# Optimization experiments

Measured on AMD Instinct MI355X. Metric: run time of the kernel, lower is better.

The kernel has to match this reference:

```python
import jax, jax.numpy as jnp
import numpy as np

B, N, C = 1, 32768, 256
NH, F, AG, P = 8, 32, 64, 4  # heads, cube side, agent tokens, pool size (P**3==AG)
HD = C // NH


def setup_inputs() -> dict:
    key = jax.random.key(0)
    ks = jax.random.split(key, 4)
    s = 0.02
    return {
        "x": jax.random.normal(ks[0], (B, N, C), jnp.float32),
        "w_qkv": jax.random.normal(ks[1], (3 * C, C), jnp.float32) * s,
        "b_qkv": jnp.zeros((3 * C,), jnp.float32),
        "w_proj": jax.random.normal(ks[2], (C, C), jnp.float32) * s,
        "b_proj": jnp.zeros((C,), jnp.float32),
        "w_dwc": jax.random.normal(ks[3], (C, C, 3, 3, 3), jnp.float32) * s,
        "b_dwc": jnp.zeros((C,), jnp.float32),
    }


def reference(x, w_qkv, b_qkv, w_proj, b_proj, w_dwc, b_dwc):
    scale = HD ** -0.5
    # qkv projection -> (3, B*NH, N, HD), replicating torch reshape/permute exactly
    qkv = x @ w_qkv.T + b_qkv                       # (B, N, 3C)
    qkv = qkv.reshape(B, N, 3, NH, HD)
    qkv = jnp.transpose(qkv, (2, 0, 3, 1, 4)).reshape(3, B * NH, N, HD)
    q, k, v = qkv[0], qkv[1], qkv[2]

    # agent tokens: pool q (note torch's raw reshape interleaves heads into channels)
    q_vol = q.reshape(B, F, F, F, C)                # faithful to torch reshape
    q_vol = jnp.transpose(q_vol, (0, 4, 1, 2, 3))   # (B, C, F, F, F)
    blk = F // P
    A = q_vol.reshape(B, C, P, blk, P, blk, P, blk).mean(axis=(3, 5, 7))  # (B,C,P,P,P)
    A = A.reshape(B, C, AG).transpose(0, 2, 1)      # (B, AG, C)
    A = A.reshape(B, AG, NH, HD).transpose(0, 2, 1, 3).reshape(B * NH, AG, HD)

    # stage 1: agents attend to keys, aggregate values
    agent_attn = jax.nn.softmax((A * scale) @ jnp.swapaxes(k, -2, -1), axis=-1)  # (B*NH, AG, N)
    agent_v = agent_attn @ v                        # (B*NH, AG, HD)
    # stage 2: queries attend to agents
    q_attn = jax.nn.softmax((q * scale) @ jnp.swapaxes(A, -2, -1), axis=-1)      # (B*NH, N, AG)
    o = q_attn @ agent_v                            # (B*NH, N, HD)

    # faithful to torch: transpose(1,2) then raw reshape
    o = jnp.swapaxes(o, 1, 2).reshape(B, N, C)

    # conv residual on v: (B*NH, N, HD) -> (B, C, F, F, F)
    v5 = jnp.swapaxes(v, 1, 2).reshape(B, C, F, F, F)
    conv = jax.lax.conv_general_dilated(
        v5, w_dwc, window_strides=(1, 1, 1), padding="SAME",
        dimension_numbers=("NCDHW", "OIDHW", "NCDHW"))
    conv = conv + b_dwc[None, :, None, None, None]
    o = o + jnp.transpose(conv, (0, 2, 3, 4, 1)).reshape(B, N, C)

    return o @ w_proj.T + b_proj
```

## Files before the change

kernel.cpp:

```cpp
#include <hip/hip_runtime.h>
#include <stdint.h>

typedef unsigned short u16;
typedef __attribute__((ext_vector_type(8))) short bf16x8;
typedef __attribute__((ext_vector_type(4))) float f32x4;

#define KSCALE (0.17677669529663687f / 512.0f)

__device__ __forceinline__ u16 f2b(float f) {
  unsigned u = __float_as_uint(f);
  unsigned r = (u + 0x7fffu + ((u >> 16) & 1u)) >> 16;
  return (u16)r;
}
__device__ __forceinline__ float b2f(u16 s) { return __uint_as_float(((unsigned)s) << 16); }

__device__ __forceinline__ void async16(const void* g, void* l) {
  __builtin_amdgcn_global_load_lds((const __attribute__((address_space(1))) unsigned int*)g,
                                   (__attribute__((address_space(3))) unsigned int*)l, 16, 0, 0);
}

__device__ __forceinline__ bf16x8 frag8(const float* p, float k) {
  float4 f0 = *(const float4*)p, f1 = *(const float4*)(p + 4);
  bf16x8 v;
  v[0] = f2b(f0.x * k); v[1] = f2b(f0.y * k); v[2] = f2b(f0.z * k); v[3] = f2b(f0.w * k);
  v[4] = f2b(f1.x * k); v[5] = f2b(f1.y * k); v[6] = f2b(f1.z * k); v[7] = f2b(f1.w * k);
  return v;
}

__global__ void prep_cast(const float* __restrict__ x, const float* __restrict__ wq,
                          const float* __restrict__ wp, const float* __restrict__ wdwc,
                          u16* __restrict__ Xb, u16* __restrict__ Wqb,
                          u16* __restrict__ Wpb, u16* __restrict__ Wc) {
  int b = blockIdx.x, tid = threadIdx.x;
  if (b < 8448) {
    const float* src; u16* dst; int i;
    if (b < 8192)      { src = x;  dst = Xb;  i = b * 256 + tid; }
    else if (b < 8384) { src = wq; dst = Wqb; i = (b - 8192) * 256 + tid; }
    else               { src = wp; dst = Wpb; i = (b - 8384) * 256 + tid; }
    const float4 v = ((const float4*)src)[i];
    uint2 o;
    o.x = (unsigned)f2b(v.x) | ((unsigned)f2b(v.y) << 16);
    o.y = (unsigned)f2b(v.z) | ((unsigned)f2b(v.w) << 16);
    ((uint2*)dst)[i] = o;
  } else {
    int o = b - 8448;
    __shared__ u16 lds[6912];
    for (int t = tid; t < 6912; t += 256) lds[t] = f2b(wdwc[o * 6912 + t]);
    __syncthreads();
    for (int idx = tid; idx < 6912; idx += 256) {
      int tp = idx >> 8, i = idx & 255;
      Wc[o * 6912 + idx] = lds[i * 27 + tp];
    }
  }
}

__global__ void prep_av(const u16* __restrict__ QKV, u16* __restrict__ v5,
                        float* __restrict__ Apre) {
  int b = blockIdx.x, tid = threadIdx.x;
  if (b < 4913) {
    int idx = b * 256 + tid;
    int c8 = idx & 31, vox = idx >> 5;
    int z = vox / 1156, r2 = vox - z * 1156, y = r2 / 34, x = r2 - y * 34;
    bf16x8 val = {0, 0, 0, 0, 0, 0, 0, 0};
    if (z >= 1 && z <= 32 && y >= 1 && y <= 32 && x >= 1 && x <= 32) {
      int n = (z - 1) * 1024 + (y - 1) * 32 + (x - 1);
      val = *(const bf16x8*)(QKV + n * 768 + 512 + c8 * 8);
    }
    *(bf16x8*)(v5 + vox * 256 + c8 * 8) = val;
  } else {
    int b2 = b - 4913;
    int a = b2 >> 3, s = b2 & 7;
    int hp = tid >> 5, dp = tid & 31;
    int p1 = a >> 4, p2 = (a >> 2) & 3, p3 = a & 3;
    float sum = 0.f;
    for (int ui = 0; ui < 64; ++ui) {
      int u = s * 64 + ui;
      int f1 = p1 * 8 + (u >> 6);
      int f2 = p2 * 8 + ((u >> 3) & 7);
      int f3 = p3 * 8 + (u & 7);
      int vox = f1 * 1024 + f2 * 32 + f3;
      int n  = ((vox & 4095) << 3) + hp;
      int cq = ((vox >> 12) << 5) + dp;
      sum += b2f(QKV[n * 768 + cq]);
    }
    atomicAdd(&Apre[(hp * 64 + a) * 32 + dp], sum);
  }
}


__device__ __forceinline__ void stage64(const u16* src, int row0, int ld, int k0,
                                        short* dst, int tid) {
  int wv = tid >> 6, lane = tid & 63;
  int r15 = lane & 15, kc8 = (lane >> 4) * 8;
#pragma unroll
  for (int j = 0; j < 4; ++j) {
    int p = j & 1, g = wv * 2 + (j >> 1);
    async16(src + (row0 + g * 16 + r15) * ld + k0 + p * 32 + kc8, dst + p * 4096 + g * 512);
  }
}

__device__ __forceinline__ void mfma64(const short* As, const short* Bs, int wm, int wn,
                                       int lane, f32x4 acc[4][4]) {
  const int q = lane >> 4, c = lane & 15;
  const int fo = q * 128 + c * 8;
#pragma unroll
  for (int p = 0; p < 2; ++p) {
    bf16x8 a[4], b[4];
#pragma unroll
    for (int mt = 0; mt < 4; ++mt) a[mt] = *(const bf16x8*)&As[p * 4096 + (wm * 4 + mt) * 512 + fo];
#pragma unroll
    for (int nt = 0; nt < 4; ++nt) b[nt] = *(const bf16x8*)&Bs[p * 4096 + (wn * 4 + nt) * 512 + fo];
#pragma unroll
    for (int mt = 0; mt < 4; ++mt)
#pragma unroll
      for (int nt = 0; nt < 4; ++nt)
        acc[mt][nt] = __builtin_amdgcn_mfma_f32_16x16x32_bf16(a[mt], b[nt], acc[mt][nt], 0, 0, 0);
  }
}

__global__ __launch_bounds__(256) void gemm_qkv(const u16* __restrict__ Xb,
                                                const u16* __restrict__ Wq,
                                                const float* __restrict__ bias,
                                                u16* __restrict__ QKV) {
  const int m0 = blockIdx.x * 128, n0 = blockIdx.y * 128;
  const int tid = threadIdx.x, lane = tid & 63, wv = tid >> 6;
  const int wm = wv >> 1, wn = wv & 1, q = lane >> 4, c = lane & 15;
  __shared__ short As[8192], Bs[8192];
  f32x4 acc[4][4] = {};
  for (int kb = 0; kb < 256; kb += 64) {
    stage64(Xb, m0, 256, kb, As, tid);
    stage64(Wq, n0, 256, kb, Bs, tid);
    __syncthreads();
    mfma64(As, Bs, wm, wn, lane, acc);
    __syncthreads();
  }
#pragma unroll
  for (int nt = 0; nt < 4; ++nt) {
    int col = n0 + wn * 64 + nt * 16 + c;
    float bv = bias[col];
#pragma unroll
    for (int mt = 0; mt < 4; ++mt) {
      int row = m0 + wm * 64 + mt * 16 + q * 4;
#pragma unroll
      for (int r = 0; r < 4; ++r) QKV[(row + r) * 768 + col] = f2b(acc[mt][nt][r] + bv);
    }
  }
}

__global__ __launch_bounds__(256) void conv_s1(const u16* __restrict__ v5,
                                               const u16* __restrict__ Wc,
                                               const float* __restrict__ bias,
                                               u16* __restrict__ Xp,
                                               const u16* __restrict__ QKV,
                                               const float* __restrict__ Apre,
                                               float* __restrict__ avac,
                                               float* __restrict__ rsum) {
  extern __shared__ char smem[];
  const int tid = threadIdx.x, lane = tid & 63, wv = tid >> 6;
  const int q = lane >> 4, c = lane & 15;
  if (blockIdx.x < 512) {
    const int bid = blockIdx.x;
    const int xcd = bid & 7, idx = bid >> 3;
    const int n0 = (idx & 1) * 128;
    const int mt_i = xcd * 32 + (idx >> 1);
    const int m0 = mt_i * 128;
    const int z0 = mt_i >> 3, y0 = (mt_i & 7) * 4;
    const int wm = wv >> 1, wn = wv & 1;
    const int r15 = lane & 15, kq8 = (lane >> 4) * 8;
    short* As = (short*)smem;
    short* Bs = (short*)(smem + 9216);
    f32x4 acc[4][4] = {};
    const u16* browB = Wc + (n0 + r15) * 6912 + kq8;
    for (int dzy = 0; dzy < 9; ++dzy) {
      int dz = dzy / 3, dy = dzy - dz * 3;
      int base = (z0 + dz) * 1156 + (y0 + dy) * 34;
      int tap0 = dzy * 3;
      for (int panel = 0; panel < 8; ++panel) {
        int choff = panel * 32 + kq8;
        for (int g = wv; g < 9; g += 4) {
          int row = base + g * 16 + r15;
          row = row < 39303 ? row : 39303;
          async16(v5 + row * 256 + choff, As + g * 512);
        }
#pragma unroll
        for (int i = wv; i < 24; i += 4) {
          int dx = i >> 3, g = i & 7;
          async16(browB + g * (16 * 6912) + (tap0 + dx) * 256 + panel * 32, Bs + i * 512);
        }
        __syncthreads();
#pragma unroll
        for (int dx = 0; dx < 3; ++dx) {
          bf16x8 a[4], b[4];
#pragma unroll
          for (int mt = 0; mt < 4; ++mt) {
            int M = wm * 64 + mt * 16 + c;
            int vx = M + 2 * (M >> 5) + dx;
            a[mt] = *(const bf16x8*)&As[(vx >> 4) * 512 + q * 128 + (vx & 15) * 8];
          }
#pragma unroll
          for (int nt = 0; nt < 4; ++nt)
            b[nt] = *(const bf16x8*)&Bs[dx * 4096 + (wn * 4 + nt) * 512 + q * 128 + c * 8];
#pragma unroll
          for (int mt = 0; mt < 4; ++mt)
#pragma unroll
            for (int nt = 0; nt < 4; ++nt)
              acc[mt][nt] = __builtin_amdgcn_mfma_f32_16x16x32_bf16(a[mt], b[nt], acc[mt][nt], 0, 0, 0);
        }
        __syncthreads();
      }
    }
#pragma unroll
    for (int nt = 0; nt < 4; ++nt) {
      int col = n0 + wn * 64 + nt * 16 + c;
      float bv = bias[col];
#pragma unroll
      for (int mt = 0; mt < 4; ++mt) {
        int row = m0 + wm * 64 + mt * 16 + q * 4;
#pragma unroll
        for (int r = 0; r < 4; ++r) Xp[(row + r) * 256 + col] = f2b(acc[mt][nt][r] + bv);
      }
    }
  } else {
    const int vb = blockIdx.x - 512;
    const int h = vb >> 7, n0 = (vb & 127) * 256;
    u16* E  = (u16*)smem;
    u16* VT = (u16*)(smem + 33792);
    float* RED = (float*)smem;
    {
      const u16* vrow = QKV + (n0 + tid) * 768 + 512 + h * 32;
#pragma unroll
      for (int d8 = 0; d8 < 4; ++d8) {
        bf16x8 v = *(const bf16x8*)(vrow + d8 * 8);
#pragma unroll
        for (int e = 0; e < 8; ++e) VT[(d8 * 8 + e) * 264 + tid] = (u16)v[e];
      }
    }
    {
      bf16x8 af[4], bf[4];
#pragma unroll
      for (int mt = 0; mt < 4; ++mt)
        af[mt] = frag8(Apre + h * 2048 + (mt * 16 + c) * 32 + q * 8, KSCALE);
#pragma unroll
      for (int nt = 0; nt < 4; ++nt)
        bf[nt] = *(const bf16x8*)(QKV + (n0 + wv * 64 + nt * 16 + c) * 768 + 256 + h * 32 + q * 8);
#pragma unroll
      for (int mt = 0; mt < 4; ++mt)
#pragma unroll
        for (int nt = 0; nt < 4; ++nt) {
          f32x4 s = {0.f, 0.f, 0.f, 0.f};
          s = __builtin_amdgcn_mfma_f32_16x16x32_bf16(af[mt], bf[nt], s, 0, 0, 0);
#pragma unroll
          for (int r = 0; r < 4; ++r) {
            int a = mt * 16 + q * 4 + r, nl = wv * 64 + nt * 16 + c;
            E[a * 264 + nl] = f2b(__expf(s[r]));
          }
        }
    }
    __syncthreads();
    {
      int a = tid >> 2, seg = tid & 3;
      float sum = 0.f;
      for (int i = 0; i < 64; ++i) sum += b2f(E[a * 264 + seg * 64 + i]);
      sum += __shfl_xor(sum, 1);
      sum += __shfl_xor(sum, 2);
      if (seg == 0) atomicAdd(&rsum[h * 64 + a], sum);
    }
    f32x4 pv[4][2] = {};
#pragma unroll
    for (int ks = 0; ks < 2; ++ks) {
      bf16x8 ap[4], bp[2];
#pragma unroll
      for (int mt = 0; mt < 4; ++mt)
        ap[mt] = *(const bf16x8*)&E[(mt * 16 + c) * 264 + wv * 64 + ks * 32 + q * 8];
#pragma unroll
      for (int nt = 0; nt < 2; ++nt)
        bp[nt] = *(const bf16x8*)&VT[(nt * 16 + c) * 264 + wv * 64 + ks * 32 + q * 8];
#pragma unroll
      for (int mt = 0; mt < 4; ++mt)
#pragma unroll
        for (int nt = 0; nt < 2; ++nt)
          pv[mt][nt] = __builtin_amdgcn_mfma_f32_16x16x32_bf16(ap[mt], bp[nt], pv[mt][nt], 0, 0, 0);
    }
    __syncthreads();
#pragma unroll
    for (int mt = 0; mt < 4; ++mt)
#pragma unroll
      for (int nt = 0; nt < 2; ++nt)
#pragma unroll
        for (int r = 0; r < 4; ++r)
          RED[wv * 2048 + (mt * 16 + q * 4 + r) * 32 + nt * 16 + c] = pv[mt][nt][r];
    __syncthreads();
    for (int idx = tid; idx < 2048; idx += 256) {
      float t = RED[idx] + RED[2048 + idx] + RED[4096 + idx] + RED[6144 + idx];
      atomicAdd(&avac[h * 2048 + idx], t);
    }
  }
}

__global__ __launch_bounds__(256) void gemm_proj(const u16* __restrict__ Xp,
                                                 const u16* __restrict__ Wp,
                                                 const float* __restrict__ bias,
                                                 float* __restrict__ out) {
  const int m0 = blockIdx.x * 128, n0 = blockIdx.y * 128;
  const int tid = threadIdx.x, lane = tid & 63, wv = tid >> 6;
  const int wm = wv >> 1, wn = wv & 1, q = lane >> 4, c = lane & 15;
  __shared__ short As[8192], Bs[8192];
  f32x4 acc[4][4] = {};
  for (int kb = 0; kb < 256; kb += 64) {
    stage64(Xp, m0, 256, kb, As, tid);
    stage64(Wp, n0, 256, kb, Bs, tid);
    __syncthreads();
    mfma64(As, Bs, wm, wn, lane, acc);
    __syncthreads();
  }
#pragma unroll
  for (int nt = 0; nt < 4; ++nt) {
    int col = n0 + wn * 64 + nt * 16 + c;
    float bv = bias[col];
#pragma unroll
    for (int mt = 0; mt < 4; ++mt) {
      int row = m0 + wm * 64 + mt * 16 + q * 4;
#pragma unroll
      for (int r = 0; r < 4; ++r) out[(row + r) * 256 + col] = acc[mt][nt][r] + bv;
    }
  }
}

__global__ __launch_bounds__(256) void s2_attn(const u16* __restrict__ QKV,
                                               const float* __restrict__ Apre,
                                               const float* __restrict__ avac,
                                               const float* __restrict__ rsum,
                                               u16* __restrict__ Xp) {
  const int h = blockIdx.y, n0 = blockIdx.x * 256;
  const int tid = threadIdx.x, lane = tid & 63, wv = tid >> 6;
  const int q = lane >> 4, c = lane & 15;
  extern __shared__ char smem[];
  u16* P = (u16*)smem;
  float* O = (float*)smem;
  u16* AVT = (u16*)(smem + 36864);

  for (int j = 0; j < 8; ++j) {
    int i = j * 256 + tid;
    int a = i >> 5, d = i & 31;
    AVT[d * 72 + a] = f2b(avac[h * 2048 + i] / rsum[h * 64 + a]);
  }

  f32x4 s[4][4];
  {
    bf16x8 af[4], bf[4];
#pragma unroll
    for (int mt = 0; mt < 4; ++mt)
      af[mt] = *(const bf16x8*)(QKV + (n0 + wv * 64 + mt * 16 + c) * 768 + h * 32 + q * 8);
#pragma unroll
    for (int nt = 0; nt < 4; ++nt)
      bf[nt] = frag8(Apre + h * 2048 + (nt * 16 + c) * 32 + q * 8, KSCALE);
#pragma unroll
    for (int mt = 0; mt < 4; ++mt)
#pragma unroll
      for (int nt = 0; nt < 4; ++nt) {
        f32x4 z = {0.f, 0.f, 0.f, 0.f};
        s[mt][nt] = __builtin_amdgcn_mfma_f32_16x16x32_bf16(af[mt], bf[nt], z, 0, 0, 0);
      }
  }
#pragma unroll
  for (int mt = 0; mt < 4; ++mt)
#pragma unroll
    for (int r = 0; r < 4; ++r) {
      float v0 = s[mt][0][r], v1 = s[mt][1][r], v2 = s[mt][2][r], v3 = s[mt][3][r];
      float mx = fmaxf(fmaxf(v0, v1), fmaxf(v2, v3));
      mx = fmaxf(mx, __shfl_xor(mx, 1));
      mx = fmaxf(mx, __shfl_xor(mx, 2));
      mx = fmaxf(mx, __shfl_xor(mx, 4));
      mx = fmaxf(mx, __shfl_xor(mx, 8));
      float e0 = __expf(v0 - mx), e1 = __expf(v1 - mx), e2 = __expf(v2 - mx), e3 = __expf(v3 - mx);
      float sm = e0 + e1 + e2 + e3;
      sm += __shfl_xor(sm, 1);
      sm += __shfl_xor(sm, 2);
      sm += __shfl_xor(sm, 4);
      sm += __shfl_xor(sm, 8);
      float inv = 1.0f / sm;
      int tok = wv * 64 + mt * 16 + q * 4 + r;
      P[tok * 72 +      c] = f2b(e0 * inv);
      P[tok * 72 + 16 + c] = f2b(e1 * inv);
      P[tok * 72 + 32 + c] = f2b(e2 * inv);
      P[tok * 72 + 48 + c] = f2b(e3 * inv);
    }
  __syncthreads();
  f32x4 o[4][2] = {};
#pragma unroll
  for (int ks = 0; ks < 2; ++ks) {
    bf16x8 ap[4], bv[2];
#pragma unroll
    for (int mt = 0; mt < 4; ++mt)
      ap[mt] = *(const bf16x8*)&P[(wv * 64 + mt * 16 + c) * 72 + ks * 32 + q * 8];
#pragma unroll
    for (int nt = 0; nt < 2; ++nt)
      bv[nt] = *(const bf16x8*)&AVT[(nt * 16 + c) * 72 + ks * 32 + q * 8];
#pragma unroll
    for (int mt = 0; mt < 4; ++mt)
#pragma unroll
      for (int nt = 0; nt < 2; ++nt)
        o[mt][nt] = __builtin_amdgcn_mfma_f32_16x16x32_bf16(ap[mt], bv[nt], o[mt][nt], 0, 0, 0);
  }
  __syncthreads();
#pragma unroll
  for (int mt = 0; mt < 4; ++mt)
#pragma unroll
    for (int nt = 0; nt < 2; ++nt)
#pragma unroll
      for (int r = 0; r < 4; ++r)
        O[(nt * 16 + c) * 258 + wv * 64 + mt * 16 + q * 4 + r] = o[mt][nt][r];
  __syncthreads();
  for (int d = 0; d < 32; ++d) {
    int addr = (h * 32 + d) * 32768 + n0 + tid;
    Xp[addr] = f2b(b2f(Xp[addr]) + O[d * 258 + tid]);
  }
}


extern "C" void kernel_launch(void* const* d_in, const int* in_sizes, int n_in,
                              void* d_out, int out_size, void* d_ws, size_t ws_size,
                              hipStream_t stream) {
  const float* x      = (const float*)d_in[0];
  const float* w_qkv  = (const float*)d_in[1];
  const float* b_qkv  = (const float*)d_in[2];
  const float* w_proj = (const float*)d_in[3];
  const float* b_proj = (const float*)d_in[4];
  const float* w_dwc  = (const float*)d_in[5];
  const float* b_dwc  = (const float*)d_in[6];
  float* out = (float*)d_out;
  char* ws = (char*)d_ws;

  u16* Xb   = (u16*)(ws);
  u16* QKV  = (u16*)(ws + 16777216);
  u16* V5   = (u16*)(ws + 67108864);
  u16* Wc   = (u16*)(ws + 87232512);
  u16* Wqb  = (u16*)(ws + 90771456);
  u16* Wpb  = (u16*)(ws + 91164672);
  float* AVAC = (float*)(ws + 91361280);
  float* RSUM = (float*)(ws + 91426816);
  float* APRE = (float*)(ws + 91428864);
  u16* Xp = Xb;

  hipMemsetAsync(AVAC, 0, 65536 + 2048 + 65536, stream);
  prep_cast<<<8704, 256, 0, stream>>>(x, w_qkv, w_proj, w_dwc, Xb, Wqb, Wpb, Wc);
  gemm_qkv<<<dim3(256, 6), 256, 0, stream>>>(Xb, Wqb, b_qkv, QKV);
  prep_av<<<5425, 256, 0, stream>>>(QKV, V5, APRE);
  conv_s1<<<2560, 256, 50688, stream>>>(V5, Wc, b_dwc, Xp, QKV, APRE, AVAC, RSUM);
  s2_attn<<<dim3(128, 8), 256, 41472, stream>>>(QKV, APRE, AVAC, RSUM, Xp);
  gemm_proj<<<dim3(256, 2), 256, 0, stream>>>(Xp, Wpb, b_proj, out);
}
```

Before: 349.1 us.

## Double-buffer conv A tiles and load pre-swizzled conv weights directly to registers

The conv-weight prep kernel now writes weights in an MFMA-fragment-friendly blocked layout, so the conv GEMM reads B fragments straight from global memory into registers instead of staging them through LDS. The A (voxel) tile is double-buffered in LDS, with the next step's async loads issued before the current step's MFMAs, leaving one barrier per step instead of two. This aims to hide global load latency and cut LDS traffic and syncs. In exchange it adds direct global loads on the critical path each step, which depend on L2 hits for the weights, and it raises register pressure.

```diff
diff --git a/kernel.cpp b/kernel.cpp
--- a/kernel.cpp
+++ b/kernel.cpp
@@ -47,9 +47,10 @@
     __shared__ u16 lds[6912];
     for (int t = tid; t < 6912; t += 256) lds[t] = f2b(wdwc[o * 6912 + t]);
     __syncthreads();
+    int ob = ((o >> 4) * 27) * 4096 + (o & 15) * 32;
     for (int idx = tid; idx < 6912; idx += 256) {
-      int tp = idx >> 8, i = idx & 255;
-      Wc[o * 6912 + idx] = lds[i * 27 + tp];
+      int t = idx >> 8, i = idx & 255;
+      Wc[ob + t * 4096 + (i >> 5) * 512 + ((i >> 3) & 3) * 8 + (i & 7)] = lds[i * 27 + t];
     }
   }
 }
@@ -167,47 +168,58 @@
     const int z0 = mt_i >> 3, y0 = (mt_i & 7) * 4;
     const int wm = wv >> 1, wn = wv & 1;
     const int r15 = lane & 15, kq8 = (lane >> 4) * 8;
-    short* As = (short*)smem;
-    short* Bs = (short*)(smem + 9216);
+    short* As0 = (short*)smem;
+    short* As1 = (short*)smem + 4608;
     f32x4 acc[4][4] = {};
-    const u16* browB = Wc + (n0 + r15) * 6912 + kq8;
-    for (int dzy = 0; dzy < 9; ++dzy) {
-      int dz = dzy / 3, dy = dzy - dz * 3;
-      int base = (z0 + dz) * 1156 + (y0 + dy) * 34;
-      int tap0 = dzy * 3;
-      for (int panel = 0; panel < 8; ++panel) {
-        int choff = panel * 32 + kq8;
+    const u16* Bq = Wc + c * 32 + q * 8;
+    const int nb = ((n0 >> 4) + wn * 4) * 27;
+    {
+      int base = z0 * 1156 + y0 * 34;
+      for (int g = wv; g < 9; g += 4) {
+        int row = base + g * 16 + r15;
+        row = row < 39303 ? row : 39303;
+        async16(v5 + row * 256 + kq8, As0 + g * 512);
+      }
+    }
+    __syncthreads();
+    short* cur = As0; short* nxt = As1;
+    for (int t = 0; t < 72; ++t) {
+      const int dzy = t >> 3, panel = t & 7;
+      const int tap0 = dzy * 3;
+      bf16x8 breg[3][4];
+#pragma unroll
+      for (int dx = 0; dx < 3; ++dx)
+#pragma unroll
+        for (int nt = 0; nt < 4; ++nt)
+          breg[dx][nt] = *(const bf16x8*)(Bq + ((nb + nt * 27 + tap0 + dx) * 8 + panel) * 512);
+      if (t < 71) {
+        const int t1 = t + 1, dzy1 = t1 >> 3, panel1 = t1 & 7;
+        const int dz1 = dzy1 / 3, dy1 = dzy1 - dz1 * 3;
+        const int base1 = (z0 + dz1) * 1156 + (y0 + dy1) * 34;
+        const int choff1 = panel1 * 32 + kq8;
         for (int g = wv; g < 9; g += 4) {
-          int row = base + g * 16 + r15;
+          int row = base1 + g * 16 + r15;
           row = row < 39303 ? row : 39303;
-          async16(v5 + row * 256 + choff, As + g * 512);
+          async16(v5 + row * 256 + choff1, nxt + g * 512);
         }
-#pragma unroll
-        for (int i = wv; i < 24; i += 4) {
-          int dx = i >> 3, g = i & 7;
-          async16(browB + g * (16 * 6912) + (tap0 + dx) * 256 + panel * 32, Bs + i * 512);
+      }
+#pragma unroll
+      for (int dx = 0; dx < 3; ++dx) {
+        bf16x8 a[4];
+#pragma unroll
+        for (int mt = 0; mt < 4; ++mt) {
+          int M = wm * 64 + mt * 16 + c;
+          int vx = M + 2 * (M >> 5) + dx;
+          a[mt] = *(const bf16x8*)&cur[(vx >> 4) * 512 + q * 128 + (vx & 15) * 8];
         }
-        __syncthreads();
-#pragma unroll
-        for (int dx = 0; dx < 3; ++dx) {
-          bf16x8 a[4], b[4];
-#pragma unroll
-          for (int mt = 0; mt < 4; ++mt) {
-            int M = wm * 64 + mt * 16 + c;
-            int vx = M + 2 * (M >> 5) + dx;
-            a[mt] = *(const bf16x8*)&As[(vx >> 4) * 512 + q * 128 + (vx & 15) * 8];
-          }
+#pragma unroll
+        for (int mt = 0; mt < 4; ++mt)
 #pragma unroll
           for (int nt = 0; nt < 4; ++nt)
-            b[nt] = *(const bf16x8*)&Bs[dx * 4096 + (wn * 4 + nt) * 512 + q * 128 + c * 8];
-#pragma unroll
-          for (int mt = 0; mt < 4; ++mt)
-#pragma unroll
-            for (int nt = 0; nt < 4; ++nt)
-              acc[mt][nt] = __builtin_amdgcn_mfma_f32_16x16x32_bf16(a[mt], b[nt], acc[mt][nt], 0, 0, 0);
-        }
-        __syncthreads();
-      }
+            acc[mt][nt] = __builtin_amdgcn_mfma_f32_16x16x32_bf16(a[mt], breg[dx][nt], acc[mt][nt], 0, 0, 0);
+      }
+      __syncthreads();
+      short* tmp = cur; cur = nxt; nxt = tmp;
     }
 #pragma unroll
     for (int nt = 0; nt < 4; ++nt) {
@@ -235,6 +247,7 @@
         for (int e = 0; e < 8; ++e) VT[(d8 * 8 + e) * 264 + tid] = (u16)v[e];
       }
     }
+    const int wv_ = tid >> 6;
     {
       bf16x8 af[4], bf[4];
 #pragma unroll
@@ -242,7 +255,7 @@
         af[mt] = frag8(Apre + h * 2048 + (mt * 16 + c) * 32 + q * 8, KSCALE);
 #pragma unroll
       for (int nt = 0; nt < 4; ++nt)
-        bf[nt] = *(const bf16x8*)(QKV + (n0 + wv * 64 + nt * 16 + c) * 768 + 256 + h * 32 + q * 8);
+        bf[nt] = *(const bf16x8*)(QKV + (n0 + wv_ * 64 + nt * 16 + c) * 768 + 256 + h * 32 + q * 8);
 #pragma unroll
       for (int mt = 0; mt < 4; ++mt)
 #pragma unroll
@@ -251,7 +264,7 @@
           s = __builtin_amdgcn_mfma_f32_16x16x32_bf16(af[mt], bf[nt], s, 0, 0, 0);
 #pragma unroll
           for (int r = 0; r < 4; ++r) {
-            int a = mt * 16 + q * 4 + r, nl = wv * 64 + nt * 16 + c;
+            int a = mt * 16 + q * 4 + r, nl = wv_ * 64 + nt * 16 + c;
             E[a * 264 + nl] = f2b(__expf(s[r]));
           }
         }
@@ -271,10 +284,10 @@
       bf16x8 ap[4], bp[2];
 #pragma unroll
       for (int mt = 0; mt < 4; ++mt)
-        ap[mt] = *(const bf16x8*)&E[(mt * 16 + c) * 264 + wv * 64 + ks * 32 + q * 8];
+        ap[mt] = *(const bf16x8*)&E[(mt * 16 + c) * 264 + wv_ * 64 + ks * 32 + q * 8];
 #pragma unroll
       for (int nt = 0; nt < 2; ++nt)
-        bp[nt] = *(const bf16x8*)&VT[(nt * 16 + c) * 264 + wv * 64 + ks * 32 + q * 8];
+        bp[nt] = *(const bf16x8*)&VT[(nt * 16 + c) * 264 + wv_ * 64 + ks * 32 + q * 8];
 #pragma unroll
       for (int mt = 0; mt < 4; ++mt)
 #pragma unroll
@@ -288,7 +301,7 @@
       for (int nt = 0; nt < 2; ++nt)
 #pragma unroll
         for (int r = 0; r < 4; ++r)
-          RED[wv * 2048 + (mt * 16 + q * 4 + r) * 32 + nt * 16 + c] = pv[mt][nt][r];
+          RED[wv_ * 2048 + (mt * 16 + q * 4 + r) * 32 + nt * 16 + c] = pv[mt][nt][r];
     __syncthreads();
     for (int idx = tid; idx < 2048; idx += 256) {
       float t = RED[idx] + RED[2048 + idx] + RED[4096 + idx] + RED[6144 + idx];
```

Result: no change. 350.0 us (+0.3%).

## Load conv operands directly from global into registers with fragment-packed weight layout

Applied to the files above, without the earlier changes.

The depthwise-style conv GEMM no longer stages activation and weight tiles through LDS with async loads and barriers. Instead, the weight tensor is pre-permuted into an MFMA-fragment-ready layout so each lane can read its bf16x8 fragment directly, and activation fragments are read straight from the padded v5 volume. This removes LDS traffic and the two syncthreads per panel, but relies on L1/L2 for reuse across waves, raises register pressure (24 fragments live), and may issue more redundant global loads.

```diff
diff --git a/kernel.cpp b/kernel.cpp
--- a/kernel.cpp
+++ b/kernel.cpp
@@ -47,9 +47,12 @@
     __shared__ u16 lds[6912];
     for (int t = tid; t < 6912; t += 256) lds[t] = f2b(wdwc[o * 6912 + t]);
     __syncthreads();
+    int o16 = o >> 4, co = o & 15;
     for (int idx = tid; idx < 6912; idx += 256) {
-      int tp = idx >> 8, i = idx & 255;
-      Wc[o * 6912 + idx] = lds[i * 27 + tp];
+      int t = idx >> 8, i = idx & 255;
+      int dz = t / 9, rem = t - dz * 9;
+      int panel = i >> 5, q = (i >> 3) & 3, e = i & 7;
+      Wc[(((panel * 3 + dz) * 16 + o16) * 9 + rem) * 512 + co * 32 + q * 8 + e] = lds[i * 27 + t];
     }
   }
 }
@@ -166,47 +169,40 @@
     const int m0 = mt_i * 128;
     const int z0 = mt_i >> 3, y0 = (mt_i & 7) * 4;
     const int wm = wv >> 1, wn = wv & 1;
-    const int r15 = lane & 15, kq8 = (lane >> 4) * 8;
-    short* As = (short*)smem;
-    short* Bs = (short*)(smem + 9216);
     f32x4 acc[4][4] = {};
-    const u16* browB = Wc + (n0 + r15) * 6912 + kq8;
+    const u16* BqB = Wc + c * 32 + q * 8;
+    const int o16b = (n0 >> 4) + wn * 4;
+    int rowb[4];
+#pragma unroll
+    for (int mt = 0; mt < 4; ++mt) {
+      int M = wm * 64 + mt * 16;
+      rowb[mt] = z0 * 1156 + (y0 + (M >> 5)) * 34 + (M & 31) + c;
+    }
     for (int dzy = 0; dzy < 9; ++dzy) {
-      int dz = dzy / 3, dy = dzy - dz * 3;
-      int base = (z0 + dz) * 1156 + (y0 + dy) * 34;
-      int tap0 = dzy * 3;
+      const int dz = dzy / 3, dy = dzy - dz * 3;
+      const int rofs = dz * 1156 + dy * 34;
+      const u16* pb = BqB + (dz * 16 + o16b) * 4608 + dy * 3 * 512;
       for (int panel = 0; panel < 8; ++panel) {
-        int choff = panel * 32 + kq8;
-        for (int g = wv; g < 9; g += 4) {
-          int row = base + g * 16 + r15;
-          row = row < 39303 ? row : 39303;
-          async16(v5 + row * 256 + choff, As + g * 512);
+        const u16* pbp = pb + panel * (3 * 16 * 4608);
+        const int cofs = panel * 32 + q * 8;
+        bf16x8 b[12], a[12];
+#pragma unroll
+        for (int dx = 0; dx < 3; ++dx) {
+#pragma unroll
+          for (int nt = 0; nt < 4; ++nt)
+            b[dx * 4 + nt] = *(const bf16x8*)(pbp + nt * 4608 + dx * 512);
+#pragma unroll
+          for (int mt = 0; mt < 4; ++mt)
+            a[dx * 4 + mt] = *(const bf16x8*)(v5 + (rowb[mt] + rofs + dx) * 256 + cofs);
         }
 #pragma unroll
-        for (int i = wv; i < 24; i += 4) {
-          int dx = i >> 3, g = i & 7;
-          async16(browB + g * (16 * 6912) + (tap0 + dx) * 256 + panel * 32, Bs + i * 512);
-        }
-        __syncthreads();
-#pragma unroll
-        for (int dx = 0; dx < 3; ++dx) {
-          bf16x8 a[4], b[4];
-#pragma unroll
-          for (int mt = 0; mt < 4; ++mt) {
-            int M = wm * 64 + mt * 16 + c;
-            int vx = M + 2 * (M >> 5) + dx;
-            a[mt] = *(const bf16x8*)&As[(vx >> 4) * 512 + q * 128 + (vx & 15) * 8];
-          }
-#pragma unroll
-          for (int nt = 0; nt < 4; ++nt)
-            b[nt] = *(const bf16x8*)&Bs[dx * 4096 + (wn * 4 + nt) * 512 + q * 128 + c * 8];
+        for (int dx = 0; dx < 3; ++dx)
 #pragma unroll
           for (int mt = 0; mt < 4; ++mt)
 #pragma unroll
             for (int nt = 0; nt < 4; ++nt)
-              acc[mt][nt] = __builtin_amdgcn_mfma_f32_16x16x32_bf16(a[mt], b[nt], acc[mt][nt], 0, 0, 0);
-        }
-        __syncthreads();
+              acc[mt][nt] = __builtin_amdgcn_mfma_f32_16x16x32_bf16(a[dx * 4 + mt], b[dx * 4 + nt],
+                                                                    acc[mt][nt], 0, 0, 0);
       }
     }
 #pragma unroll
@@ -235,6 +231,7 @@
         for (int e = 0; e < 8; ++e) VT[(d8 * 8 + e) * 264 + tid] = (u16)v[e];
       }
     }
+    const int wv_ = tid >> 6;
     {
       bf16x8 af[4], bf[4];
 #pragma unroll
@@ -242,7 +239,7 @@
         af[mt] = frag8(Apre + h * 2048 + (mt * 16 + c) * 32 + q * 8, KSCALE);
 #pragma unroll
       for (int nt = 0; nt < 4; ++nt)
-        bf[nt] = *(const bf16x8*)(QKV + (n0 + wv * 64 + nt * 16 + c) * 768 + 256 + h * 32 + q * 8);
+        bf[nt] = *(const bf16x8*)(QKV + (n0 + wv_ * 64 + nt * 16 + c) * 768 + 256 + h * 32 + q * 8);
 #pragma unroll
       for (int mt = 0; mt < 4; ++mt)
 #pragma unroll
@@ -251,7 +248,7 @@
           s = __builtin_amdgcn_mfma_f32_16x16x32_bf16(af[mt], bf[nt], s, 0, 0, 0);
 #pragma unroll
           for (int r = 0; r < 4; ++r) {
-            int a = mt * 16 + q * 4 + r, nl = wv * 64 + nt * 16 + c;
+            int a = mt * 16 + q * 4 + r, nl = wv_ * 64 + nt * 16 + c;
             E[a * 264 + nl] = f2b(__expf(s[r]));
           }
         }
@@ -271,10 +268,10 @@
       bf16x8 ap[4], bp[2];
 #pragma unroll
       for (int mt = 0; mt < 4; ++mt)
-        ap[mt] = *(const bf16x8*)&E[(mt * 16 + c) * 264 + wv * 64 + ks * 32 + q * 8];
+        ap[mt] = *(const bf16x8*)&E[(mt * 16 + c) * 264 + wv_ * 64 + ks * 32 + q * 8];
 #pragma unroll
       for (int nt = 0; nt < 2; ++nt)
-        bp[nt] = *(const bf16x8*)&VT[(nt * 16 + c) * 264 + wv * 64 + ks * 32 + q * 8];
+        bp[nt] = *(const bf16x8*)&VT[(nt * 16 + c) * 264 + wv_ * 64 + ks * 32 + q * 8];
 #pragma unroll
       for (int mt = 0; mt < 4; ++mt)
 #pragma unroll
@@ -288,7 +285,7 @@
       for (int nt = 0; nt < 2; ++nt)
 #pragma unroll
         for (int r = 0; r < 4; ++r)
-          RED[wv * 2048 + (mt * 16 + q * 4 + r) * 32 + nt * 16 + c] = pv[mt][nt][r];
+          RED[wv_ * 2048 + (mt * 16 + q * 4 + r) * 32 + nt * 16 + c] = pv[mt][nt][r];
     __syncthreads();
     for (int idx = tid; idx < 2048; idx += 256) {
       float t = RED[idx] + RED[2048 + idx] + RED[4096 + idx] + RED[6144 + idx];
```

Measured after the change: 510.0 us. +46.1%, slower.
